# Performance work log

Hardware: AMD Instinct MI355X
Metric: run time of the kernel (lower is better)

The kernel has to match this reference:

```python
import jax, jax.numpy as jnp
import numpy as np
from jax import lax

T, B, E = 4096, 8, 512


def setup_inputs() -> dict:
    key = jax.random.key(0)
    k1, k2, k3 = jax.random.split(key, 3)
    x = jax.random.normal(k1, (T, B, E), dtype=jnp.float32)
    raw_pos_beta = jax.random.normal(k2, (E,), dtype=jnp.float32)
    raw_neg_beta = jax.random.normal(k3, (E,), dtype=jnp.float32)
    return {"x": x, "raw_pos_beta": raw_pos_beta, "raw_neg_beta": raw_neg_beta}


def reference(x, raw_pos_beta, raw_neg_beta):
    # pos/neg split EMA. The torch module computes out[t] = sum_{s<=t} beta^(t-s) u[s]
    # via a length-T depthwise conv; that is exactly the linear recurrence
    # mem[t] = beta * mem[t-1] + u[t], which we run as an O(T) scan.
    pos_beta = jax.nn.sigmoid(raw_pos_beta)  # [E]
    neg_beta = jax.nn.sigmoid(raw_neg_beta)  # [E]
    x_pos = jnp.where(x >= 0, x, 0.0) * (1.0 - pos_beta)  # [T,B,E]
    x_neg = jnp.where(x <= 0, x, 0.0) * (1.0 - neg_beta)  # [T,B,E]
    u = jnp.stack([x_pos, x_neg], axis=-1)                # [T,B,E,2]
    beta = jnp.stack([pos_beta, neg_beta], axis=-1)       # [E,2]

    def step(carry, u_t):
        new = beta * carry + u_t  # [B,E,2]
        return new, new

    init = jnp.zeros(u.shape[1:], dtype=x.dtype)
    _, mem2 = lax.scan(step, init, u)  # [T,B,E,2]
    return mem2[..., 0] + mem2[..., 1]  # [T,B,E]
```

## Files before the change

### kernel.cpp

```cpp
#include <hip/hip_runtime.h>


#define T_DIM 4096
#define B_DIM 8
#define E_DIM 512
#define CHUNK_L 64
#define NCHUNK (T_DIM / CHUNK_L)
#define BE (B_DIM * E_DIM)

__device__ __forceinline__ float sigmoidf_(float x) { return 1.0f / (1.0f + __expf(-x)); }
__device__ __forceinline__ float pow64_(float b) {
    float t = b * b; t *= t; t *= t; t *= t; t *= t; t *= t; return t;
}

__global__ __launch_bounds__(256) void k_agg(
        const float* __restrict__ x,
        const float* __restrict__ rp,
        const float* __restrict__ rn,
        float* __restrict__ agg) {
    const int gtid = blockIdx.x * 256 + threadIdx.x;
    const int q = gtid & 1023;
    const int c = gtid >> 10;
    const int e = (q & 127) * 4;
    const int b = q >> 7;
    const int col = b * E_DIM + e;

    float4 rp4 = *(const float4*)(rp + e);
    float4 rn4 = *(const float4*)(rn + e);
    float bp[4] = {sigmoidf_(rp4.x), sigmoidf_(rp4.y), sigmoidf_(rp4.z), sigmoidf_(rp4.w)};
    float bn[4] = {sigmoidf_(rn4.x), sigmoidf_(rn4.y), sigmoidf_(rn4.z), sigmoidf_(rn4.w)};

    float fp[4] = {0.f, 0.f, 0.f, 0.f};
    float fn[4] = {0.f, 0.f, 0.f, 0.f};
    const size_t xbase = (size_t)c * CHUNK_L * BE + col;
    #pragma unroll 8
    for (int k = 0; k < CHUNK_L; k++) {
        float4 xv = *(const float4*)(x + xbase + (size_t)k * BE);
        float f[4] = {xv.x, xv.y, xv.z, xv.w};
        #pragma unroll
        for (int j = 0; j < 4; j++) {
            fp[j] = bp[j] * fp[j] + fmaxf(f[j], 0.f) * (1.0f - bp[j]);
            fn[j] = bn[j] * fn[j] + fminf(f[j], 0.f) * (1.0f - bn[j]);
        }
    }
    *(float4*)(agg + (size_t)(c * 2 + 0) * BE + col) = make_float4(fp[0], fp[1], fp[2], fp[3]);
    *(float4*)(agg + (size_t)(c * 2 + 1) * BE + col) = make_float4(fn[0], fn[1], fn[2], fn[3]);
}

__global__ __launch_bounds__(256) void ParallelDLIEMA_17789754541002_kernel(
        const float* __restrict__ x,
        const float* __restrict__ rp,
        const float* __restrict__ rn,
        const float* __restrict__ agg,
        float* __restrict__ out) {
    const int gtid = blockIdx.x * 256 + threadIdx.x;
    const int q = gtid & 1023;
    const int c = gtid >> 10;
    const int e = (q & 127) * 4;
    const int b = q >> 7;
    const int col = b * E_DIM + e;

    float4 rp4 = *(const float4*)(rp + e);
    float4 rn4 = *(const float4*)(rn + e);
    float bp[4] = {sigmoidf_(rp4.x), sigmoidf_(rp4.y), sigmoidf_(rp4.z), sigmoidf_(rp4.w)};
    float bn[4] = {sigmoidf_(rn4.x), sigmoidf_(rn4.y), sigmoidf_(rn4.z), sigmoidf_(rn4.w)};

    float Ap[4], An[4];
    #pragma unroll
    for (int j = 0; j < 4; j++) { Ap[j] = pow64_(bp[j]); An[j] = pow64_(bn[j]); }

    float sp[4] = {0.f, 0.f, 0.f, 0.f};
    float sn[4] = {0.f, 0.f, 0.f, 0.f};
    #pragma unroll 4
    for (int j = 0; j < c; ++j) {
        float4 ap = *(const float4*)(agg + (size_t)(j * 2 + 0) * BE + col);
        float4 an = *(const float4*)(agg + (size_t)(j * 2 + 1) * BE + col);
        sp[0] = Ap[0] * sp[0] + ap.x;  sn[0] = An[0] * sn[0] + an.x;
        sp[1] = Ap[1] * sp[1] + ap.y;  sn[1] = An[1] * sn[1] + an.y;
        sp[2] = Ap[2] * sp[2] + ap.z;  sn[2] = An[2] * sn[2] + an.z;
        sp[3] = Ap[3] * sp[3] + ap.w;  sn[3] = An[3] * sn[3] + an.w;
    }

    const size_t xbase = (size_t)c * CHUNK_L * BE + col;
    #pragma unroll 8
    for (int k = 0; k < CHUNK_L; k++) {
        float4 xv = *(const float4*)(x + xbase + (size_t)k * BE);
        float f[4] = {xv.x, xv.y, xv.z, xv.w};
        float o[4];
        #pragma unroll
        for (int j = 0; j < 4; j++) {
            sp[j] = bp[j] * sp[j] + fmaxf(f[j], 0.f) * (1.0f - bp[j]);
            sn[j] = bn[j] * sn[j] + fminf(f[j], 0.f) * (1.0f - bn[j]);
            o[j] = sp[j] + sn[j];
        }
        *(float4*)(out + xbase + (size_t)k * BE) = make_float4(o[0], o[1], o[2], o[3]);
    }
}


#define FB_CHUNK_L 16
#define FB_NCHUNK (T_DIM / FB_CHUNK_L)

__global__ __launch_bounds__(256) void k1_local(
        const float* __restrict__ x, const float* __restrict__ rp,
        const float* __restrict__ rn, float* __restrict__ out) {
    int gtid = blockIdx.x * 256 + threadIdx.x;
    int e4 = gtid & 127; int b = (gtid >> 7) & 7; int c = gtid >> 10; int e = e4 * 4;
    float4 rp4 = *(const float4*)(rp + e);
    float4 rn4 = *(const float4*)(rn + e);
    float bp[4] = {sigmoidf_(rp4.x), sigmoidf_(rp4.y), sigmoidf_(rp4.z), sigmoidf_(rp4.w)};
    float bn[4] = {sigmoidf_(rn4.x), sigmoidf_(rn4.y), sigmoidf_(rn4.z), sigmoidf_(rn4.w)};
    float fp4[4] = {0.f,0.f,0.f,0.f}, fn4[4] = {0.f,0.f,0.f,0.f};
    int base = c * FB_CHUNK_L * BE + b * E_DIM + e;
    #pragma unroll
    for (int k = 0; k < FB_CHUNK_L; k++) {
        float4 xv = *(const float4*)(x + base + k * BE);
        float f[4] = {xv.x, xv.y, xv.z, xv.w};
        #pragma unroll
        for (int j = 0; j < 4; j++) {
            fp4[j] = bp[j] * fp4[j] + fmaxf(f[j], 0.f) * (1.0f - bp[j]);
            fn4[j] = bn[j] * fn4[j] + fminf(f[j], 0.f) * (1.0f - bn[j]);
        }
    }
    *(float4*)(out + base + 0 * BE) = make_float4(fp4[0], fp4[1], fp4[2], fp4[3]);
    *(float4*)(out + base + 1 * BE) = make_float4(fn4[0], fn4[1], fn4[2], fn4[3]);
}

__global__ __launch_bounds__(256) void k_carry(const float* __restrict__ rp,
                                               const float* __restrict__ rn,
                                               float* __restrict__ out) {
    int gtid = blockIdx.x * 256 + threadIdx.x;
    int e = gtid & 511; int b = (gtid >> 9) & 7; int s = gtid >> 12;
    float beta = sigmoidf_(s ? rn[e] : rp[e]);
    float bl = beta * beta; bl = bl * bl; bl = bl * bl; bl = bl * bl;
    float* p = out + s * BE + b * E_DIM + e;
    float carry = 0.f;
    for (int g = 0; g < FB_NCHUNK / 16; g++) {
        float fv[16];
        #pragma unroll
        for (int u = 0; u < 16; u++) fv[u] = p[(g * 16 + u) * (FB_CHUNK_L * BE)];
        #pragma unroll
        for (int u = 0; u < 16; u++) {
            p[(g * 16 + u) * (FB_CHUNK_L * BE)] = carry;
            carry = bl * carry + fv[u];
        }
    }
}

__global__ __launch_bounds__(256) void k_out(const float* __restrict__ x,
                                             const float* __restrict__ rp,
                                             const float* __restrict__ rn,
                                             float* __restrict__ out) {
    int gtid = blockIdx.x * 256 + threadIdx.x;
    int e4 = gtid & 127; int b = (gtid >> 7) & 7; int c = gtid >> 10; int e = e4 * 4;
    float4 rp4 = *(const float4*)(rp + e);
    float4 rn4 = *(const float4*)(rn + e);
    float bp[4] = {sigmoidf_(rp4.x), sigmoidf_(rp4.y), sigmoidf_(rp4.z), sigmoidf_(rp4.w)};
    float bn[4] = {sigmoidf_(rn4.x), sigmoidf_(rn4.y), sigmoidf_(rn4.z), sigmoidf_(rn4.w)};
    int base = c * FB_CHUNK_L * BE + b * E_DIM + e;
    float4 cp = *(const float4*)(out + base + 0 * BE);
    float4 cn = *(const float4*)(out + base + 1 * BE);
    float lp[4] = {cp.x, cp.y, cp.z, cp.w};
    float ln[4] = {cn.x, cn.y, cn.z, cn.w};
    #pragma unroll
    for (int k = 0; k < FB_CHUNK_L; k++) {
        float4 xv = *(const float4*)(x + base + k * BE);
        float f[4] = {xv.x, xv.y, xv.z, xv.w};
        float o[4];
        #pragma unroll
        for (int j = 0; j < 4; j++) {
            lp[j] = bp[j] * lp[j] + fmaxf(f[j], 0.f) * (1.0f - bp[j]);
            ln[j] = bn[j] * ln[j] + fminf(f[j], 0.f) * (1.0f - bn[j]);
            o[j] = lp[j] + ln[j];
        }
        *(float4*)(out + base + k * BE) = make_float4(o[0], o[1], o[2], o[3]);
    }
}

extern "C" void kernel_launch(void* const* d_in, const int* in_sizes, int n_in,
                              void* d_out, int out_size, void* d_ws, size_t ws_size,
                              hipStream_t stream) {
    const float* x  = (const float*)d_in[0];
    const float* rp = (const float*)d_in[1];
    const float* rn = (const float*)d_in[2];
    float* out = (float*)d_out;

    const size_t need = (size_t)2 * NCHUNK * BE * sizeof(float);
    if (d_ws != nullptr && ws_size >= need) {
        float* agg = (float*)d_ws;
        k_agg<<<256, 256, 0, stream>>>(x, rp, rn, agg);
        ParallelDLIEMA_17789754541002_kernel<<<256, 256, 0, stream>>>(x, rp, rn, agg, out);
    } else {
        k1_local<<<1024, 256, 0, stream>>>(x, rp, rn, out);
        k_carry<<<32, 256, 0, stream>>>(rp, rn, out);
        k_out<<<1024, 256, 0, stream>>>(x, rp, rn, out);
    }
}
```

Baseline: 132.4 us.

## Halve chunk length and split output pass into half-chunks with mid-chunk aggregates

Shrinks the chunk length from 64 to 32, doubling the k_agg grid, and records an additional half-chunk aggregate so the output kernel can launch two threads per chunk, each covering 16 timesteps. The aim is more parallelism and occupancy (1024 blocks instead of 256) with shorter serial recurrences per thread. In exchange, each output thread's prefix scan over prior chunk aggregates doubles in length, reading more aggregate data (quadratic total), and the workspace needed grows to double-size aggregate buffers.

```diff
diff --git a/kernel.cpp b/kernel.cpp
--- a/kernel.cpp
+++ b/kernel.cpp
@@ -4,20 +4,25 @@
 #define T_DIM 4096
 #define B_DIM 8
 #define E_DIM 512
-#define CHUNK_L 64
+#define CHUNK_L 32
+#define HALF_L 16
 #define NCHUNK (T_DIM / CHUNK_L)
 #define BE (B_DIM * E_DIM)
 
 __device__ __forceinline__ float sigmoidf_(float x) { return 1.0f / (1.0f + __expf(-x)); }
-__device__ __forceinline__ float pow64_(float b) {
-    float t = b * b; t *= t; t *= t; t *= t; t *= t; t *= t; return t;
+__device__ __forceinline__ float pow32_(float b) {
+    float t = b * b; t *= t; t *= t; t *= t; t *= t; return t;
+}
+__device__ __forceinline__ float pow16_(float b) {
+    float t = b * b; t *= t; t *= t; t *= t; return t;
 }
 
 __global__ __launch_bounds__(256) void k_agg(
         const float* __restrict__ x,
         const float* __restrict__ rp,
         const float* __restrict__ rn,
-        float* __restrict__ agg) {
+        float* __restrict__ agg,
+        float* __restrict__ aggH) {
     const int gtid = blockIdx.x * 256 + threadIdx.x;
     const int q = gtid & 1023;
     const int c = gtid >> 10;
@@ -32,8 +37,9 @@
 
     float fp[4] = {0.f, 0.f, 0.f, 0.f};
     float fn[4] = {0.f, 0.f, 0.f, 0.f};
+    float hp[4], hn[4];
     const size_t xbase = (size_t)c * CHUNK_L * BE + col;
-    #pragma unroll 8
+    #pragma unroll
     for (int k = 0; k < CHUNK_L; k++) {
         float4 xv = *(const float4*)(x + xbase + (size_t)k * BE);
         float f[4] = {xv.x, xv.y, xv.z, xv.w};
@@ -42,9 +48,15 @@
             fp[j] = bp[j] * fp[j] + fmaxf(f[j], 0.f) * (1.0f - bp[j]);
             fn[j] = bn[j] * fn[j] + fminf(f[j], 0.f) * (1.0f - bn[j]);
         }
-    }
-    *(float4*)(agg + (size_t)(c * 2 + 0) * BE + col) = make_float4(fp[0], fp[1], fp[2], fp[3]);
-    *(float4*)(agg + (size_t)(c * 2 + 1) * BE + col) = make_float4(fn[0], fn[1], fn[2], fn[3]);
+        if (k == HALF_L - 1) {
+            #pragma unroll
+            for (int j = 0; j < 4; j++) { hp[j] = fp[j]; hn[j] = fn[j]; }
+        }
+    }
+    *(float4*)(agg  + (size_t)(c * 2 + 0) * BE + col) = make_float4(fp[0], fp[1], fp[2], fp[3]);
+    *(float4*)(agg  + (size_t)(c * 2 + 1) * BE + col) = make_float4(fn[0], fn[1], fn[2], fn[3]);
+    *(float4*)(aggH + (size_t)(c * 2 + 0) * BE + col) = make_float4(hp[0], hp[1], hp[2], hp[3]);
+    *(float4*)(aggH + (size_t)(c * 2 + 1) * BE + col) = make_float4(hn[0], hn[1], hn[2], hn[3]);
 }
 
 __global__ __launch_bounds__(256) void ParallelDLIEMA_17789754541002_kernel(
@@ -52,10 +64,13 @@
         const float* __restrict__ rp,
         const float* __restrict__ rn,
         const float* __restrict__ agg,
+        const float* __restrict__ aggH,
         float* __restrict__ out) {
     const int gtid = blockIdx.x * 256 + threadIdx.x;
-    const int q = gtid & 1023;
-    const int c = gtid >> 10;
+    const int q  = gtid & 1023;
+    const int ch = gtid >> 10;
+    const int h  = ch & 1;
+    const int c  = ch >> 1;
     const int e = (q & 127) * 4;
     const int b = q >> 7;
     const int col = b * E_DIM + e;
@@ -67,7 +82,7 @@
 
     float Ap[4], An[4];
     #pragma unroll
-    for (int j = 0; j < 4; j++) { Ap[j] = pow64_(bp[j]); An[j] = pow64_(bn[j]); }
+    for (int j = 0; j < 4; j++) { Ap[j] = pow32_(bp[j]); An[j] = pow32_(bn[j]); }
 
     float sp[4] = {0.f, 0.f, 0.f, 0.f};
     float sn[4] = {0.f, 0.f, 0.f, 0.f};
@@ -81,9 +96,21 @@
         sp[3] = Ap[3] * sp[3] + ap.w;  sn[3] = An[3] * sn[3] + an.w;
     }
 
-    const size_t xbase = (size_t)c * CHUNK_L * BE + col;
-    #pragma unroll 8
-    for (int k = 0; k < CHUNK_L; k++) {
+    if (h) {
+        float4 hp = *(const float4*)(aggH + (size_t)(c * 2 + 0) * BE + col);
+        float4 hn = *(const float4*)(aggH + (size_t)(c * 2 + 1) * BE + col);
+        float hpv[4] = {hp.x, hp.y, hp.z, hp.w};
+        float hnv[4] = {hn.x, hn.y, hn.z, hn.w};
+        #pragma unroll
+        for (int j = 0; j < 4; j++) {
+            sp[j] = pow16_(bp[j]) * sp[j] + hpv[j];
+            sn[j] = pow16_(bn[j]) * sn[j] + hnv[j];
+        }
+    }
+
+    const size_t xbase = ((size_t)c * CHUNK_L + (size_t)h * HALF_L) * BE + col;
+    #pragma unroll
+    for (int k = 0; k < HALF_L; k++) {
         float4 xv = *(const float4*)(x + xbase + (size_t)k * BE);
         float f[4] = {xv.x, xv.y, xv.z, xv.w};
         float o[4];
@@ -185,11 +212,13 @@
     const float* rn = (const float*)d_in[2];
     float* out = (float*)d_out;
 
-    const size_t need = (size_t)2 * NCHUNK * BE * sizeof(float);
+    const size_t aggN = (size_t)2 * NCHUNK * BE;
+    const size_t need = 2 * aggN * sizeof(float);
     if (d_ws != nullptr && ws_size >= need) {
-        float* agg = (float*)d_ws;
-        k_agg<<<256, 256, 0, stream>>>(x, rp, rn, agg);
-        ParallelDLIEMA_17789754541002_kernel<<<256, 256, 0, stream>>>(x, rp, rn, agg, out);
+        float* agg  = (float*)d_ws;
+        float* aggH = agg + aggN;
+        k_agg<<<512, 256, 0, stream>>>(x, rp, rn, agg, aggH);
+        ParallelDLIEMA_17789754541002_kernel<<<1024, 256, 0, stream>>>(x, rp, rn, agg, aggH, out);
     } else {
         k1_local<<<1024, 256, 0, stream>>>(x, rp, rn, out);
         k_carry<<<32, 256, 0, stream>>>(rp, rn, out);
```

New measurement: 136.2 us. 2.9% more time.
